# Kernel tuning notes

Hardware: AMD Instinct MI355X
Metric: run time of the kernel (lower is better)

Reference implementation:

```python
import jax, jax.numpy as jnp
import numpy as np

DIM = 768
NUM_HEADS = 12

def setup_inputs() -> dict:
    key = jax.random.key(0)
    ks = jax.random.split(key, 8)
    B, N, C = 16, 3136, DIM
    x = jax.random.normal(ks[0], (B, N, C), dtype=jnp.float32)
    # nn.Linear(dim, 3*dim): y = x @ W^T + b; store W already transposed [C, 3C]
    qkv_w = jax.random.normal(ks[1], (C, 3 * C), dtype=jnp.float32) * (C ** -0.5)
    qkv_b = jax.random.normal(ks[2], (3 * C,), dtype=jnp.float32) * 0.02
    # depthwise Conv2d(dim, dim, 3, padding=1, groups=dim): kernel OIHW [C,1,3,3]
    dw_w = jax.random.normal(ks[3], (C, 1, 3, 3), dtype=jnp.float32) * (1.0 / 3.0)
    dw_b = jax.random.normal(ks[4], (C,), dtype=jnp.float32) * 0.02
    proj_w = jax.random.normal(ks[5], (C, C), dtype=jnp.float32) * (C ** -0.5)
    proj_b = jax.random.normal(ks[6], (C,), dtype=jnp.float32) * 0.02
    return {"x": x, "qkv_w": qkv_w, "qkv_b": qkv_b, "dw_w": dw_w,
            "dw_b": dw_b, "proj_w": proj_w, "proj_b": proj_b}

def reference(x, qkv_w, qkv_b, dw_w, dw_b, proj_w, proj_b):
    B, N, C = x.shape
    H = NUM_HEADS
    d = C // H
    scale = d ** -0.5
    qkv = (x @ qkv_w + qkv_b).reshape(B, N, 3, H, d).transpose(2, 0, 3, 1, 4)
    q, k, v = qkv[0], qkv[1], qkv[2]  # each [B,H,N,d]
    q = jax.nn.relu(q) * scale
    k = jax.nn.relu(k)
    # linear attention: context = k^T @ v  -> [B,H,d,d]
    context = jnp.einsum('bhnd,bhne->bhde', k, v)
    out = jnp.einsum('bhnd,bhde->bhne', q, context)  # [B,H,N,d]
    out = out.transpose(0, 2, 1, 3).reshape(B, N, C)
    hw = int(N ** 0.5)  # N is a perfect square token grid
    img = out.transpose(0, 2, 1).reshape(B, C, hw, hw)
    img = jax.lax.conv_general_dilated(
        img, dw_w, window_strides=(1, 1), padding='SAME',
        feature_group_count=C,
        dimension_numbers=('NCHW', 'OIHW', 'NCHW')) + dw_b[None, :, None, None]
    out = img.reshape(B, C, N).transpose(0, 2, 1)
    return out @ proj_w + proj_b
```

## Files before the change

### kernel.cpp

```cpp
#include <hip/hip_runtime.h>

typedef unsigned short ushort_t;
typedef __attribute__((ext_vector_type(8))) short short8;
typedef __attribute__((ext_vector_type(4))) float f32x4;

#define DEV __device__ __forceinline__

DEV unsigned short f2bf(float f) {
  unsigned int u = __float_as_uint(f);
  u += 0x7FFFu + ((u >> 16) & 1u);
  return (unsigned short)(u >> 16);
}
DEV float bf2f(unsigned short h) { return __uint_as_float(((unsigned int)h) << 16); }

DEV void gload_lds16(const void* g, void* l) {
  __builtin_amdgcn_global_load_lds((const __attribute__((address_space(1))) void*)g,
                                   (__attribute__((address_space(3))) void*)l, 16, 0, 0);
}

__global__ void cvt_x_k(const float4* __restrict__ in, ushort4* __restrict__ out) {
  const int i = blockIdx.x * 256 + threadIdx.x;
  float4 f = in[i];
  out[i] = make_ushort4(f2bf(f.x), f2bf(f.y), f2bf(f.z), f2bf(f.w));
}

__global__ __launch_bounds__(256)
void transp_k(const float* __restrict__ in, ushort_t* __restrict__ out, int R, int Cn) {
  __shared__ float tile[32][33];
  const int ctiles = Cn >> 5;
  const int bx = blockIdx.x % ctiles;
  const int by = blockIdx.x / ctiles;
  const int tx = threadIdx.x & 31, ty = threadIdx.x >> 5;
  #pragma unroll
  for (int i = 0; i < 4; ++i) {
    const int r = by * 32 + ty + i * 8;
    tile[ty + i * 8][tx] = in[(size_t)r * Cn + bx * 32 + tx];
  }
  __syncthreads();
  #pragma unroll
  for (int i = 0; i < 4; ++i) {
    const int cc = bx * 32 + ty + i * 8;
    out[(size_t)cc * R + by * 32 + tx] = f2bf(tile[tx][ty + i * 8]);
  }
}

template <int MODE>
__global__ __launch_bounds__(512, 2)
void gemm256(const ushort_t* __restrict__ A, const ushort_t* __restrict__ BT,
             const float* __restrict__ bias,
             void* __restrict__ o0, void* __restrict__ o1, void* __restrict__ o2,
             int K, int ntiles) {
  __shared__ __attribute__((aligned(16))) ushort_t As[2][16384];
  __shared__ __attribute__((aligned(16))) ushort_t Bs[2][16384];

  const int nwg = gridDim.x;
  const int qq = nwg >> 3, rr = nwg & 7;
  const int xcd = blockIdx.x & 7;
  const int idx = blockIdx.x >> 3;
  const int bid = (xcd < rr ? xcd * (qq + 1) : rr * (qq + 1) + (xcd - rr) * qq) + idx;
  const int nt = bid % ntiles, mt = bid / ntiles;

  const int t = threadIdx.x;
  const int w = t >> 6, l = t & 63;
  const int wr = w >> 2, wc = w & 3;
  const int lr = l & 15, lg = l >> 4;

  const ushort_t* Ap = A + (size_t)mt * 256 * K;
  const ushort_t* Bp = BT + (size_t)nt * 256 * K;

  const int srow = t >> 3;
  const int scb  = (t & 7) * 16;
  const int gcb = scb ^ ((srow & 7) << 4);

  f32x4 acc[8][4];
  #pragma unroll
  for (int i = 0; i < 8; ++i)
    #pragma unroll
    for (int j = 0; j < 4; ++j) acc[i][j] = (f32x4){0.f, 0.f, 0.f, 0.f};

  const int NT = K >> 6;

  #pragma unroll
  for (int j = 0; j < 4; ++j) {
    const int row = j * 64 + srow;
    gload_lds16(Ap + (size_t)row * K + (gcb >> 1), &As[0][row * 64 + (scb >> 1)]);
    gload_lds16(Bp + (size_t)row * K + (gcb >> 1), &Bs[0][row * 64 + (scb >> 1)]);
  }
  __syncthreads();

  for (int kt = 0; kt < NT; ++kt) {
    const int cur = kt & 1;
    if (kt + 1 < NT) {
      const int k0 = (kt + 1) << 6;
      #pragma unroll
      for (int j = 0; j < 4; ++j) {
        const int row = j * 64 + srow;
        gload_lds16(Ap + (size_t)row * K + k0 + (gcb >> 1),
                    &As[cur ^ 1][row * 64 + (scb >> 1)]);
        gload_lds16(Bp + (size_t)row * K + k0 + (gcb >> 1),
                    &Bs[cur ^ 1][row * 64 + (scb >> 1)]);
      }
    }
    short8 bf[4][2];
    #pragma unroll
    for (int nf = 0; nf < 4; ++nf) {
      const int rb = wc * 64 + nf * 16 + lr;
      const int xr = (rb & 7) << 4;
      #pragma unroll
      for (int ks = 0; ks < 2; ++ks) {
        const int kb = ks * 64 + lg * 16;
        bf[nf][ks] = *(const short8*)&Bs[cur][rb * 64 + ((kb ^ xr) >> 1)];
      }
    }
    #pragma unroll
    for (int qm = 0; qm < 2; ++qm) {
      short8 af[4][2];
      #pragma unroll
      for (int mf = 0; mf < 4; ++mf) {
        const int ra = wr * 128 + qm * 64 + mf * 16 + lr;
        const int xr = (ra & 7) << 4;
        #pragma unroll
        for (int ks = 0; ks < 2; ++ks) {
          const int kb = ks * 64 + lg * 16;
          af[mf][ks] = *(const short8*)&As[cur][ra * 64 + ((kb ^ xr) >> 1)];
        }
      }
      __builtin_amdgcn_s_setprio(1);
      #pragma unroll
      for (int mf = 0; mf < 4; ++mf)
        #pragma unroll
        for (int nf = 0; nf < 4; ++nf)
          #pragma unroll
          for (int ks = 0; ks < 2; ++ks)
            acc[qm * 4 + mf][nf] = __builtin_amdgcn_mfma_f32_16x16x32_bf16(
                af[mf][ks], bf[nf][ks], acc[qm * 4 + mf][nf], 0, 0, 0);
      __builtin_amdgcn_s_setprio(0);
    }
    __syncthreads();
  }

  if (MODE == 0) {
    ushort_t* q  = (ushort_t*)o0;
    ushort_t* kT = (ushort_t*)o1;
    ushort_t* vT = (ushort_t*)o2;
    #pragma unroll
    for (int nf = 0; nf < 4; ++nf) {
      const int c3 = nt * 256 + wc * 64 + nf * 16 + lr;
      const float bv = bias[c3];
      const int s = (c3 >= 1536) ? 2 : (c3 >= 768 ? 1 : 0);
      const int rem = c3 - s * 768;
      const int h = rem >> 6, dd = rem & 63;
      #pragma unroll
      for (int mi = 0; mi < 8; ++mi) {
        const int mbase = mt * 256 + wr * 128 + mi * 16 + lg * 4;
        #pragma unroll
        for (int r = 0; r < 4; ++r) {
          const int m = mbase + r;
          const int b_ = m / 3136;
          const int n = m - b_ * 3136;
          float v = acc[mi][nf][r] + bv;
          if (s == 0) {
            v = fmaxf(v, 0.f) * 0.125f;
            q[(((size_t)b_ * 12 + h) * 3136 + n) * 64 + dd] = f2bf(v);
          } else if (s == 1) {
            v = fmaxf(v, 0.f);
            kT[(((size_t)b_ * 12 + h) * 64 + dd) * 3136 + n] = f2bf(v);
          } else {
            vT[(((size_t)b_ * 12 + h) * 64 + dd) * 3136 + n] = f2bf(v);
          }
        }
      }
    }
  } else {
    float* O = (float*)o0;
    #pragma unroll
    for (int nf = 0; nf < 4; ++nf) {
      const int c = nt * 256 + wc * 64 + nf * 16 + lr;
      const float bv = bias[c];
      #pragma unroll
      for (int mi = 0; mi < 8; ++mi) {
        const int mbase = mt * 256 + wr * 128 + mi * 16 + lg * 4;
        #pragma unroll
        for (int r = 0; r < 4; ++r)
          O[(size_t)(mbase + r) * 768 + c] = acc[mi][nf][r] + bv;
      }
    }
  }
}

__global__ __launch_bounds__(64)
void ctx_k(const ushort_t* __restrict__ kT, const ushort_t* __restrict__ vT,
           float* __restrict__ ctxT) {
  __shared__ __attribute__((aligned(16))) ushort_t Ks[64 * 64];
  __shared__ __attribute__((aligned(16))) ushort_t Vs[64 * 64];
  const int bid = blockIdx.x;
  const int s = bid % 7, bh = bid / 7;
  const int n0 = s * 448;
  const int t = threadIdx.x;
  const int lr = t & 15, lg = t >> 4;
  const ushort_t* kp = kT + (size_t)bh * 64 * 3136;
  const ushort_t* vp = vT + (size_t)bh * 64 * 3136;
  const int srow = t >> 3, scol = (t & 7) * 8;

  f32x4 acc[4][4];
  #pragma unroll
  for (int i = 0; i < 4; ++i)
    #pragma unroll
    for (int j = 0; j < 4; ++j) acc[i][j] = (f32x4){0.f, 0.f, 0.f, 0.f};

  for (int c = 0; c < 7; ++c) {
    const int nb = n0 + c * 64;
    #pragma unroll
    for (int i = 0; i < 8; ++i) {
      gload_lds16(kp + (size_t)(i * 8 + srow) * 3136 + nb + scol, &Ks[(i * 8 + srow) * 64 + scol]);
      gload_lds16(vp + (size_t)(i * 8 + srow) * 3136 + nb + scol, &Vs[(i * 8 + srow) * 64 + scol]);
    }
    __syncthreads();
    #pragma unroll
    for (int kk = 0; kk < 2; ++kk) {
      short8 a[4], bfr[4];
      #pragma unroll
      for (int mf = 0; mf < 4; ++mf)
        a[mf] = *(const short8*)&Ks[(mf * 16 + lr) * 64 + kk * 32 + lg * 8];
      #pragma unroll
      for (int nf = 0; nf < 4; ++nf)
        bfr[nf] = *(const short8*)&Vs[(nf * 16 + lr) * 64 + kk * 32 + lg * 8];
      #pragma unroll
      for (int mf = 0; mf < 4; ++mf)
        #pragma unroll
        for (int nf = 0; nf < 4; ++nf)
          acc[mf][nf] = __builtin_amdgcn_mfma_f32_16x16x32_bf16(a[mf], bfr[nf], acc[mf][nf], 0, 0, 0);
    }
    __syncthreads();
  }
  float* cp = ctxT + (size_t)bh * 4096;
  #pragma unroll
  for (int mf = 0; mf < 4; ++mf)
    #pragma unroll
    for (int nf = 0; nf < 4; ++nf)
      #pragma unroll
      for (int r = 0; r < 4; ++r)
        atomicAdd(&cp[(nf * 16 + lr) * 64 + mf * 16 + lg * 4 + r], acc[mf][nf][r]);
}

__global__ __launch_bounds__(256)
void attnout_k(const ushort_t* __restrict__ q, const float* __restrict__ ctxT,
               ushort_t* __restrict__ out) {
  __shared__ __attribute__((aligned(16))) ushort_t Qs[256 * 64];
  __shared__ __attribute__((aligned(16))) ushort_t Cs[64 * 64];
  const int bid = blockIdx.x;
  const int tile = bid % 13, bh = bid / 13;
  const int b_ = bh / 12, h = bh - b_ * 12;
  const int n0 = tile * 256;
  const int t = threadIdx.x;
  const int w = t >> 6, l = t & 63;
  const int lr = l & 15, lg = l >> 4;
  const ushort_t* qp = q + (size_t)bh * 3136 * 64;

  {
    const float4* cp = (const float4*)(ctxT + (size_t)bh * 4096);
    #pragma unroll
    for (int i = 0; i < 4; ++i) {
      const int j = i * 256 + t;
      float4 f = cp[j];
      ((ushort4*)Cs)[j] = make_ushort4(f2bf(f.x), f2bf(f.y), f2bf(f.z), f2bf(f.w));
    }
  }
  const int srow = t >> 3, scol = (t & 7) * 8;
  #pragma unroll
  for (int i = 0; i < 8; ++i)
    gload_lds16(qp + (size_t)(n0 + i * 32 + srow) * 64 + scol, &Qs[(i * 32 + srow) * 64 + scol]);
  __syncthreads();

  f32x4 acc[4][4];
  #pragma unroll
  for (int i = 0; i < 4; ++i)
    #pragma unroll
    for (int j = 0; j < 4; ++j) acc[i][j] = (f32x4){0.f, 0.f, 0.f, 0.f};

  #pragma unroll
  for (int kk = 0; kk < 2; ++kk) {
    short8 a[4], bfr[4];
    #pragma unroll
    for (int mf = 0; mf < 4; ++mf)
      a[mf] = *(const short8*)&Qs[(w * 64 + mf * 16 + lr) * 64 + kk * 32 + lg * 8];
    #pragma unroll
    for (int nf = 0; nf < 4; ++nf)
      bfr[nf] = *(const short8*)&Cs[(nf * 16 + lr) * 64 + kk * 32 + lg * 8];
    #pragma unroll
    for (int mf = 0; mf < 4; ++mf)
      #pragma unroll
      for (int nf = 0; nf < 4; ++nf)
        acc[mf][nf] = __builtin_amdgcn_mfma_f32_16x16x32_bf16(a[mf], bfr[nf], acc[mf][nf], 0, 0, 0);
  }

  ushort_t* op = out + (size_t)b_ * 3136 * 768 + h * 64;
  #pragma unroll
  for (int mf = 0; mf < 4; ++mf) {
    const int nb = n0 + w * 64 + mf * 16 + lg * 4;
    #pragma unroll
    for (int r = 0; r < 4; ++r) {
      const int n = nb + r;
      if (n < 3136) {
        #pragma unroll
        for (int nf = 0; nf < 4; ++nf)
          op[(size_t)n * 768 + nf * 16 + lr] = f2bf(acc[mf][nf][r]);
      }
    }
  }
}

__global__ __launch_bounds__(768)
void dwconv_k(const ushort_t* __restrict__ in, const float* __restrict__ w9,
              const float* __restrict__ wb, ushort_t* __restrict__ out) {
  const int bn = blockIdx.x;
  const int b_ = bn / 3136, n = bn - b_ * 3136;
  const int y = n / 56, x = n - y * 56;
  const int c = threadIdx.x;
  const ushort_t* ip = in + (size_t)b_ * 3136 * 768 + c;
  float wv[9];
  #pragma unroll
  for (int i = 0; i < 9; ++i) wv[i] = w9[c * 9 + i];
  float acc = wb[c];
  #pragma unroll
  for (int dy = 0; dy < 3; ++dy) {
    const int yy = y + dy - 1;
    if ((unsigned)yy < 56u) {
      #pragma unroll
      for (int dx = 0; dx < 3; ++dx) {
        const int xx = x + dx - 1;
        if ((unsigned)xx < 56u)
          acc += bf2f(ip[(size_t)(yy * 56 + xx) * 768]) * wv[dy * 3 + dx];
      }
    }
  }
  out[(size_t)bn * 768 + c] = f2bf(acc);
}

extern "C" void kernel_launch(void* const* d_in, const int* in_sizes, int n_in,
                              void* d_out, int out_size, void* d_ws, size_t ws_size,
                              hipStream_t stream) {
  (void)in_sizes; (void)n_in; (void)out_size; (void)ws_size;
  const float* x      = (const float*)d_in[0];
  const float* qkv_w  = (const float*)d_in[1];
  const float* qkv_b  = (const float*)d_in[2];
  const float* dw_w   = (const float*)d_in[3];
  const float* dw_b   = (const float*)d_in[4];
  const float* proj_w = (const float*)d_in[5];
  const float* proj_b = (const float*)d_in[6];
  float* out = (float*)d_out;

  char* ws = (char*)d_ws;
  const size_t SZ = (size_t)50176 * 768 * 2;
  ushort_t* xbf  = (ushort_t*)(ws);
  ushort_t* attn = xbf;
  ushort_t* q    = (ushort_t*)(ws + SZ);
  ushort_t* cvo  = q;
  ushort_t* kT   = (ushort_t*)(ws + 2 * SZ);
  ushort_t* vT   = (ushort_t*)(ws + 3 * SZ);
  ushort_t* wt1  = (ushort_t*)(ws + 4 * SZ);
  ushort_t* wt2  = (ushort_t*)(ws + 4 * SZ + 3538944);
  float*    ctx  = (float*)(ws + 4 * SZ + 3538944 + 1179648);

  hipMemsetAsync(ctx, 0, (size_t)192 * 4096 * 4, stream);
  cvt_x_k<<<37632, 256, 0, stream>>>((const float4*)x, (ushort4*)xbf);
  transp_k<<<1728, 256, 0, stream>>>(qkv_w, wt1, 768, 2304);
  transp_k<<<576, 256, 0, stream>>>(proj_w, wt2, 768, 768);
  gemm256<0><<<196 * 9, 512, 0, stream>>>(xbf, wt1, qkv_b, q, kT, vT, 768, 9);
  ctx_k<<<192 * 7, 64, 0, stream>>>(kT, vT, ctx);
  attnout_k<<<192 * 13, 256, 0, stream>>>(q, ctx, attn);
  dwconv_k<<<50176, 768, 0, stream>>>(attn, dw_w, dw_b, cvo);
  gemm256<1><<<196 * 3, 512, 0, stream>>>(cvo, wt2, proj_b, out, nullptr, nullptr, 768, 3);
}
```

Measured before the change: 1.133 ms.

## Triple-buffer GEMM K-loop with BK=32 and row-sliding dwconv

```diff
diff --git a/kernel.cpp b/kernel.cpp
--- a/kernel.cpp
+++ b/kernel.cpp
@@ -46,12 +46,12 @@
 
 template <int MODE>
 __global__ __launch_bounds__(512, 2)
-void gemm256(const ushort_t* __restrict__ A, const ushort_t* __restrict__ BT,
-             const float* __restrict__ bias,
-             void* __restrict__ o0, void* __restrict__ o1, void* __restrict__ o2,
-             int K, int ntiles) {
-  __shared__ __attribute__((aligned(16))) ushort_t As[2][16384];
-  __shared__ __attribute__((aligned(16))) ushort_t Bs[2][16384];
+void gemm256p(const ushort_t* __restrict__ A, const ushort_t* __restrict__ BT,
+              const float* __restrict__ bias,
+              void* __restrict__ o0, void* __restrict__ o1, void* __restrict__ o2,
+              int K, int ntiles) {
+  __shared__ __attribute__((aligned(16))) ushort_t As[3][256 * 32];
+  __shared__ __attribute__((aligned(16))) ushort_t Bs[3][256 * 32];
 
   const int nwg = gridDim.x;
   const int qq = nwg >> 3, rr = nwg & 7;
@@ -68,9 +68,9 @@
   const ushort_t* Ap = A + (size_t)mt * 256 * K;
   const ushort_t* Bp = BT + (size_t)nt * 256 * K;
 
-  const int srow = t >> 3;
-  const int scb  = (t & 7) * 16;
-  const int gcb = scb ^ ((srow & 7) << 4);
+  const int srow = t >> 2;
+  const int scb  = (t & 3) * 16;
+  const int gcb  = scb ^ ((srow & 3) << 4);
 
   f32x4 acc[8][4];
   #pragma unroll
@@ -78,66 +78,63 @@
     #pragma unroll
     for (int j = 0; j < 4; ++j) acc[i][j] = (f32x4){0.f, 0.f, 0.f, 0.f};
 
-  const int NT = K >> 6;
-
-  #pragma unroll
-  for (int j = 0; j < 4; ++j) {
-    const int row = j * 64 + srow;
-    gload_lds16(Ap + (size_t)row * K + (gcb >> 1), &As[0][row * 64 + (scb >> 1)]);
-    gload_lds16(Bp + (size_t)row * K + (gcb >> 1), &Bs[0][row * 64 + (scb >> 1)]);
-  }
-  __syncthreads();
+  const int NT = K >> 5;
+
+#define STAGE_TILE(SLOT, KT)                                                     \
+  {                                                                              \
+    const int k0_ = (KT) << 5;                                                   \
+    _Pragma("unroll")                                                            \
+    for (int j = 0; j < 2; ++j) {                                                \
+      const int row_ = j * 128 + srow;                                           \
+      gload_lds16(Ap + (size_t)row_ * K + k0_ + (gcb >> 1),                      \
+                  &As[SLOT][row_ * 32 + (scb >> 1)]);                            \
+      gload_lds16(Bp + (size_t)row_ * K + k0_ + (gcb >> 1),                      \
+                  &Bs[SLOT][row_ * 32 + (scb >> 1)]);                            \
+    }                                                                            \
+  }
+
+  STAGE_TILE(0, 0);
+  STAGE_TILE(1, 1);
 
   for (int kt = 0; kt < NT; ++kt) {
-    const int cur = kt & 1;
-    if (kt + 1 < NT) {
-      const int k0 = (kt + 1) << 6;
-      #pragma unroll
-      for (int j = 0; j < 4; ++j) {
-        const int row = j * 64 + srow;
-        gload_lds16(Ap + (size_t)row * K + k0 + (gcb >> 1),
-                    &As[cur ^ 1][row * 64 + (scb >> 1)]);
-        gload_lds16(Bp + (size_t)row * K + k0 + (gcb >> 1),
-                    &Bs[cur ^ 1][row * 64 + (scb >> 1)]);
-      }
-    }
-    short8 bf[4][2];
+    if (kt < NT - 1) {
+      asm volatile("s_waitcnt vmcnt(4)" ::: "memory");
+    } else {
+      asm volatile("s_waitcnt vmcnt(0)" ::: "memory");
+    }
+    __builtin_amdgcn_s_barrier();
+    __builtin_amdgcn_sched_barrier(0);
+
+    const int sl = kt % 3;
+    if (kt + 2 < NT) {
+      const int s2 = (kt + 2) % 3;
+      STAGE_TILE(s2, kt + 2);
+    }
+
+    short8 bfr[4];
     #pragma unroll
     for (int nf = 0; nf < 4; ++nf) {
       const int rb = wc * 64 + nf * 16 + lr;
-      const int xr = (rb & 7) << 4;
-      #pragma unroll
-      for (int ks = 0; ks < 2; ++ks) {
-        const int kb = ks * 64 + lg * 16;
-        bf[nf][ks] = *(const short8*)&Bs[cur][rb * 64 + ((kb ^ xr) >> 1)];
-      }
-    }
-    #pragma unroll
-    for (int qm = 0; qm < 2; ++qm) {
-      short8 af[4][2];
-      #pragma unroll
-      for (int mf = 0; mf < 4; ++mf) {
-        const int ra = wr * 128 + qm * 64 + mf * 16 + lr;
-        const int xr = (ra & 7) << 4;
-        #pragma unroll
-        for (int ks = 0; ks < 2; ++ks) {
-          const int kb = ks * 64 + lg * 16;
-          af[mf][ks] = *(const short8*)&As[cur][ra * 64 + ((kb ^ xr) >> 1)];
-        }
-      }
-      __builtin_amdgcn_s_setprio(1);
-      #pragma unroll
-      for (int mf = 0; mf < 4; ++mf)
-        #pragma unroll
-        for (int nf = 0; nf < 4; ++nf)
-          #pragma unroll
-          for (int ks = 0; ks < 2; ++ks)
-            acc[qm * 4 + mf][nf] = __builtin_amdgcn_mfma_f32_16x16x32_bf16(
-                af[mf][ks], bf[nf][ks], acc[qm * 4 + mf][nf], 0, 0, 0);
-      __builtin_amdgcn_s_setprio(0);
-    }
-    __syncthreads();
-  }
+      bfr[nf] = *(const short8*)&Bs[sl][rb * 32 + (((lg * 16) ^ ((rb & 3) << 4)) >> 1)];
+    }
+    short8 af[8];
+    #pragma unroll
+    for (int mi = 0; mi < 8; ++mi) {
+      const int ra = wr * 128 + mi * 16 + lr;
+      af[mi] = *(const short8*)&As[sl][ra * 32 + (((lg * 16) ^ ((ra & 3) << 4)) >> 1)];
+    }
+
+    __builtin_amdgcn_s_setprio(1);
+    #pragma unroll
+    for (int mi = 0; mi < 8; ++mi)
+      #pragma unroll
+      for (int nf = 0; nf < 4; ++nf)
+        acc[mi][nf] = __builtin_amdgcn_mfma_f32_16x16x32_bf16(af[mi], bfr[nf],
+                                                              acc[mi][nf], 0, 0, 0);
+    __builtin_amdgcn_s_setprio(0);
+    __builtin_amdgcn_sched_barrier(0);
+  }
+#undef STAGE_TILE
 
   if (MODE == 0) {
     ushort_t* q  = (ushort_t*)o0;
@@ -310,31 +307,49 @@
   }
 }
 
-__global__ __launch_bounds__(768)
+__global__ __launch_bounds__(384)
 void dwconv_k(const ushort_t* __restrict__ in, const float* __restrict__ w9,
               const float* __restrict__ wb, ushort_t* __restrict__ out) {
-  const int bn = blockIdx.x;
-  const int b_ = bn / 3136, n = bn - b_ * 3136;
-  const int y = n / 56, x = n - y * 56;
-  const int c = threadIdx.x;
-  const ushort_t* ip = in + (size_t)b_ * 3136 * 768 + c;
-  float wv[9];
-  #pragma unroll
-  for (int i = 0; i < 9; ++i) wv[i] = w9[c * 9 + i];
-  float acc = wb[c];
-  #pragma unroll
-  for (int dy = 0; dy < 3; ++dy) {
-    const int yy = y + dy - 1;
-    if ((unsigned)yy < 56u) {
-      #pragma unroll
-      for (int dx = 0; dx < 3; ++dx) {
-        const int xx = x + dx - 1;
-        if ((unsigned)xx < 56u)
-          acc += bf2f(ip[(size_t)(yy * 56 + xx) * 768]) * wv[dy * 3 + dx];
-      }
-    }
-  }
-  out[(size_t)bn * 768 + c] = f2bf(acc);
+  const int by = blockIdx.x;
+  const int b_ = by / 56, y = by - b_ * 56;
+  const int c0 = threadIdx.x * 2;
+  const ushort_t* ip = in + (size_t)b_ * 3136 * 768;
+  ushort_t* op = out + ((size_t)b_ * 3136 + (size_t)y * 56) * 768 + c0;
+
+  float w0[9], w1[9];
+  #pragma unroll
+  for (int i = 0; i < 9; ++i) { w0[i] = w9[c0 * 9 + i]; w1[i] = w9[c0 * 9 + 9 + i]; }
+  const float bb0 = wb[c0], bb1 = wb[c0 + 1];
+
+  const int ym = y - 1, yp = y + 1;
+  const bool ymok = (ym >= 0), ypok = (yp < 56);
+  const size_t r0 = ymok ? ((size_t)(ym * 56) * 768 + c0) : 0;
+  const size_t r1 = (size_t)(y * 56) * 768 + c0;
+  const size_t r2 = ypok ? ((size_t)(yp * 56) * 768 + c0) : 0;
+
+  auto ld = [&](size_t rbase, bool ok, int xx) -> float2 {
+    if (!ok || xx >= 56) return make_float2(0.f, 0.f);
+    const unsigned int u = *(const unsigned int*)(ip + rbase + (size_t)xx * 768);
+    return make_float2(bf2f((ushort_t)(u & 0xffffu)), bf2f((ushort_t)(u >> 16)));
+  };
+
+  float2 a0 = make_float2(0.f, 0.f), a1 = ld(r0, ymok, 0), a2 = ld(r0, ymok, 1);
+  float2 b0 = make_float2(0.f, 0.f), b1 = ld(r1, true, 0), b2 = ld(r1, true, 1);
+  float2 c0v = make_float2(0.f, 0.f), c1 = ld(r2, ypok, 0), c2 = ld(r2, ypok, 1);
+
+  for (int x = 0; x < 56; ++x) {
+    float s0 = bb0 + a0.x * w0[0] + a1.x * w0[1] + a2.x * w0[2]
+                   + b0.x * w0[3] + b1.x * w0[4] + b2.x * w0[5]
+                   + c0v.x * w0[6] + c1.x * w0[7] + c2.x * w0[8];
+    float s1 = bb1 + a0.y * w1[0] + a1.y * w1[1] + a2.y * w1[2]
+                   + b0.y * w1[3] + b1.y * w1[4] + b2.y * w1[5]
+                   + c0v.y * w1[6] + c1.y * w1[7] + c2.y * w1[8];
+    *(unsigned int*)(op + (size_t)x * 768) =
+        ((unsigned int)f2bf(s1) << 16) | (unsigned int)f2bf(s0);
+    a0 = a1; a1 = a2; a2 = ld(r0, ymok, x + 2);
+    b0 = b1; b1 = b2; b2 = ld(r1, true, x + 2);
+    c0v = c1; c1 = c2; c2 = ld(r2, ypok, x + 2);
+  }
 }
 
 extern "C" void kernel_launch(void* const* d_in, const int* in_sizes, int n_in,
@@ -366,9 +381,9 @@
   cvt_x_k<<<37632, 256, 0, stream>>>((const float4*)x, (ushort4*)xbf);
   transp_k<<<1728, 256, 0, stream>>>(qkv_w, wt1, 768, 2304);
   transp_k<<<576, 256, 0, stream>>>(proj_w, wt2, 768, 768);
-  gemm256<0><<<196 * 9, 512, 0, stream>>>(xbf, wt1, qkv_b, q, kT, vT, 768, 9);
+  gemm256p<0><<<196 * 9, 512, 0, stream>>>(xbf, wt1, qkv_b, q, kT, vT, 768, 9);
   ctx_k<<<192 * 7, 64, 0, stream>>>(kT, vT, ctx);
   attnout_k<<<192 * 13, 256, 0, stream>>>(q, ctx, attn);
-  dwconv_k<<<50176, 768, 0, stream>>>(attn, dw_w, dw_b, cvo);
-  gemm256<1><<<196 * 3, 512, 0, stream>>>(cvo, wt2, proj_b, out, nullptr, nullptr, 768, 3);
-}
+  dwconv_k<<<896, 384, 0, stream>>>(attn, dw_w, dw_b, cvo);
+  gemm256p<1><<<196 * 3, 512, 0, stream>>>(cvo, wt2, proj_b, out, nullptr, nullptr, 768, 3);
+}
```

After: 1.031 ms. 9.0% less time.
